# Optimization experiments

Measured on AMD Instinct MI355X. Metric: run time of the kernel, lower is better.

Reference implementation:

```python
import jax, jax.numpy as jnp
import numpy as np
import math

SEQ_LEN = 2048
DIM = 4096
N_HEADS = 32
N_KV_HEADS = 8
HEAD_DIM = DIM // N_HEADS  # 128
ROPE_THETA = 500000.0
W_SCALE = 0.02


def _precompute_freqs(head_dim, end, theta=ROPE_THETA):
    freq = 1.0 / theta ** (jnp.arange(0, head_dim, 2, dtype=jnp.float32) / head_dim)  # [hd/2]
    t = jnp.arange(end, dtype=jnp.float32)
    f = t[:, None] * freq[None, :]  # [S, hd/2]
    return jnp.cos(f), jnp.sin(f)


def _apply_rope(x, cos, sin):
    # x: [S, H, hd]; interleaved even/odd rotation, matching torch ::2 / 1::2 indexing
    xe = x[:, :, 0::2]
    xo = x[:, :, 1::2]
    c = cos[:, None, :]  # [S, 1, hd/2]
    s = sin[:, None, :]
    re = xe * c - xo * s
    ro = xe * s + xo * c
    # re-interleave: out[..., 2i] = re[..., i], out[..., 2i+1] = ro[..., i]
    return jnp.stack([re, ro], axis=-1).reshape(x.shape)


def setup_inputs() -> dict:
    key = jax.random.key(0)
    k = jax.random.split(key, 5)
    x = jax.random.normal(k[0], (SEQ_LEN, DIM), dtype=jnp.float32)
    wq = jax.random.normal(k[1], (DIM, DIM), dtype=jnp.float32) * W_SCALE
    wk = jax.random.normal(k[2], (N_KV_HEADS * HEAD_DIM, DIM), dtype=jnp.float32) * W_SCALE
    wv = jax.random.normal(k[3], (N_KV_HEADS * HEAD_DIM, DIM), dtype=jnp.float32) * W_SCALE
    wo = jax.random.normal(k[4], (DIM, DIM), dtype=jnp.float32) * W_SCALE
    return {"x": x, "wq": wq, "wk": wk, "wv": wv, "wo": wo}


def reference(x, wq, wk, wv, wo):
    S = SEQ_LEN
    rep = N_HEADS // N_KV_HEADS  # 4

    Q = (x @ wq.T).reshape(S, N_HEADS, HEAD_DIM)
    K = (x @ wk.T).reshape(S, N_KV_HEADS, HEAD_DIM)
    V = (x @ wv.T).reshape(S, N_KV_HEADS, HEAD_DIM)

    cos, sin = _precompute_freqs(HEAD_DIM, S)
    Q = _apply_rope(Q, cos, sin)
    K = _apply_rope(K, cos, sin)

    # GQA: repeat_interleave(K, rep, dim=1) maps query head h -> kv group h // rep.
    # Express natively with a grouped einsum instead of materializing repeated K/V.
    Qg = Q.transpose(1, 0, 2).reshape(N_KV_HEADS, rep, S, HEAD_DIM)  # [g, r, S, d]
    Kt = K.transpose(1, 0, 2)  # [g, S, d]
    Vt = V.transpose(1, 0, 2)  # [g, S, d]

    scores = jnp.einsum('grqd,gkd->grqk', Qg, Kt) / math.sqrt(HEAD_DIM)
    mask = jnp.triu(jnp.full((S, S), -jnp.inf, dtype=scores.dtype), k=1)
    probs = jax.nn.softmax(scores + mask, axis=-1)
    out = jnp.einsum('grqk,gkd->grqd', probs, Vt)  # [g, r, S, d]

    out = out.reshape(N_HEADS, S, HEAD_DIM).transpose(1, 0, 2).reshape(S, N_HEADS * HEAD_DIM)
    return out @ wo.T
```

## Files before the change

### kernel.cpp

```cpp
#include <hip/hip_runtime.h>

typedef unsigned short u16;
typedef short short8 __attribute__((ext_vector_type(8)));
typedef float f32x4 __attribute__((ext_vector_type(4)));
typedef unsigned short u16x4 __attribute__((ext_vector_type(4)));

typedef short8 short8_a __attribute__((may_alias));
typedef f32x4 f32x4_a __attribute__((may_alias));
typedef u16x4 u16x4_a __attribute__((may_alias));
typedef unsigned int uint_a __attribute__((may_alias));

__device__ __forceinline__ u16 f2b(float f) {
  unsigned u = __float_as_uint(f);
  u += 0x7FFFu + ((u >> 16) & 1u);
  return (u16)(u >> 16);
}

__device__ __forceinline__ void mfma_b(f32x4& d, short8 a, short8 b) {
  asm("v_mfma_f32_16x16x32_bf16 %0, %1, %2, %0" : "+v"(d) : "v"(a), "v"(b));
}

__device__ __forceinline__ void guard4(f32x4& a, f32x4& b, f32x4& c, f32x4& d) {
  asm volatile("s_nop 7\n\ts_nop 7" : "+v"(a), "+v"(b), "+v"(c), "+v"(d));
}
__device__ __forceinline__ void guard8(f32x4* o) {
  asm volatile("s_nop 7\n\ts_nop 7"
               : "+v"(o[0]), "+v"(o[1]), "+v"(o[2]), "+v"(o[3]),
                 "+v"(o[4]), "+v"(o[5]), "+v"(o[6]), "+v"(o[7]));
}

__device__ __forceinline__ void gload16(const void* g, void* l) {
  __builtin_amdgcn_global_load_lds((__attribute__((address_space(1))) void*)(g),
                                   (__attribute__((address_space(3))) void*)(l),
                                   16, 0, 0);
}

__device__ __forceinline__ void bar_v0() {
  asm volatile("s_waitcnt vmcnt(0)\n\ts_barrier" ::: "memory");
}
__device__ __forceinline__ void bar_v3() {
  asm volatile("s_waitcnt vmcnt(3)\n\ts_barrier" ::: "memory");
}

__global__ __launch_bounds__(256)
void k_prep(const float* __restrict__ x, const float* __restrict__ wq,
            const float* __restrict__ wk, const float* __restrict__ wv,
            const float* __restrict__ wo, u16* __restrict__ xb,
            u16* __restrict__ wB, u16* __restrict__ wob,
            float* __restrict__ cost, float* __restrict__ sint) {
  const long i = (long)blockIdx.x * 256 + threadIdx.x;
  const float* src;
  u16* dst;
  long j;
  if (i < 6291456) {
    if (i < 2097152) { src = x; dst = xb; j = i; }
    else { src = wq; dst = wB; j = i - 2097152; }
  } else if (i < 8388608) {
    if (i < 7340032) { src = wk; dst = wB + 16777216; j = i - 6291456; }
    else { src = wv; dst = wB + 20971520; j = i - 7340032; }
  } else if (i < 12582912) {
    src = wo; dst = wob; j = i - 8388608;
  } else {
    long ti = i - 12582912;
    int s = (int)(ti >> 6), jj = (int)(ti & 63);
    float freq = powf(500000.0f, -(float)jj * (1.0f / 64.0f));
    float a = (float)s * freq;
    float sv, cv;
    sincosf(a, &sv, &cv);
    cost[ti] = cv;
    sint[ti] = sv;
    return;
  }
  f32x4 v = ((const f32x4_a*)src)[j];
  u16x4 o;
  o[0] = f2b(v[0]); o[1] = f2b(v[1]); o[2] = f2b(v[2]); o[3] = f2b(v[3]);
  ((u16x4_a*)dst)[j] = o;
}

#define QK_SCALE 0.08838834764831845f
__global__ __launch_bounds__(512, 2)
void k_gemm8(const u16* __restrict__ A, const u16* __restrict__ B,
             const float* __restrict__ cost, const float* __restrict__ sint,
             u16* __restrict__ Qb, u16* __restrict__ Kb, u16* __restrict__ Vt) {
  extern __shared__ u16 lds[];
  const int K = 4096;
  const int tid = threadIdx.x;
  const int w = tid >> 6, lane = tid & 63;
  const int hi = lane >> 4, lo = lane & 15;
  const int wr = w >> 2, wc = w & 3;
  int bid = blockIdx.x;
  bid = (bid & 7) * 24 + (bid >> 3);
  const int tm = bid / 24, tn = bid - (bid / 24) * 24;
  const int m0 = tm << 8, n0 = tn << 8;

  const int kx = (((tid & 7) ^ ((tid >> 3) & 7)) << 3);
  const int r3 = tid >> 3;

  f32x4 acc[8][4] = {};
  short8 afr[4][2], bfr[4][2];

  const int sA0 = (wr * 128 + lo) * 64;
  const int sB0 = (wc * 64 + lo) * 64;
  const int sl0 = ((0 * 4 + hi) ^ (lo & 7)) * 8;
  const int sl1 = ((1 * 4 + hi) ^ (lo & 7)) * 8;

#define STAGE_A(sbuf, h, kt)                                                    \
  {                                                                             \
    _Pragma("unroll") for (int l = 0; l < 2; ++l) {                             \
      gload16(A + (long)(m0 + (h)*128 + l * 64 + r3) * K + (kt)*64 + kx,        \
              lds + (sbuf)*16384 + ((h)*128 + l * 64 + w * 8) * 64);            \
    }                                                                           \
  }
#define STAGE_B(sbuf, h, kt)                                                    \
  {                                                                             \
    _Pragma("unroll") for (int l = 0; l < 2; ++l) {                             \
      gload16(B + (long)(n0 + (h)*128 + l * 64 + r3) * K + (kt)*64 + kx,        \
              lds + 32768 + (sbuf)*16384 + ((h)*128 + l * 64 + w * 8) * 64);    \
    }                                                                           \
  }

  STAGE_A(0, 0, 0); STAGE_A(0, 1, 0);
  STAGE_B(0, 0, 0); STAGE_B(0, 1, 0);
  bar_v0();

  const int NI = K >> 7;
#define HALF_ITER(buf, stile, sbuf, dostage)                                    \
  {                                                                             \
    const u16* Ab_ = lds + (buf)*16384;                                         \
    const u16* Bb_ = lds + 32768 + (buf)*16384;                                 \
    if (dostage) { STAGE_A(sbuf, 0, stile); STAGE_A(sbuf, 1, stile); }          \
    _Pragma("unroll") for (int fn = 0; fn < 4; ++fn) {                          \
      bfr[fn][0] = *(const short8_a*)(Bb_ + sB0 + fn * 1024 + sl0);             \
      bfr[fn][1] = *(const short8_a*)(Bb_ + sB0 + fn * 1024 + sl1);             \
    }                                                                           \
    _Pragma("unroll") for (int fm = 0; fm < 4; ++fm) {                          \
      afr[fm][0] = *(const short8_a*)(Ab_ + sA0 + fm * 1024 + sl0);             \
      afr[fm][1] = *(const short8_a*)(Ab_ + sA0 + fm * 1024 + sl1);             \
    }                                                                           \
    __builtin_amdgcn_s_setprio(1);                                              \
    _Pragma("unroll") for (int fm = 0; fm < 4; ++fm)                            \
      _Pragma("unroll") for (int fn = 0; fn < 4; ++fn) {                        \
        mfma_b(acc[fm][fn], afr[fm][0], bfr[fn][0]);                            \
        mfma_b(acc[fm][fn], afr[fm][1], bfr[fn][1]);                            \
      }                                                                         \
    __builtin_amdgcn_s_setprio(0);                                              \
    if (dostage) { STAGE_B(sbuf, 0, stile); STAGE_B(sbuf, 1, stile); }          \
    _Pragma("unroll") for (int fm = 0; fm < 4; ++fm) {                          \
      afr[fm][0] = *(const short8_a*)(Ab_ + sA0 + (fm + 4) * 1024 + sl0);       \
      afr[fm][1] = *(const short8_a*)(Ab_ + sA0 + (fm + 4) * 1024 + sl1);       \
    }                                                                           \
    __builtin_amdgcn_s_setprio(1);                                              \
    _Pragma("unroll") for (int fm = 0; fm < 4; ++fm)                            \
      _Pragma("unroll") for (int fn = 0; fn < 4; ++fn) {                        \
        mfma_b(acc[fm + 4][fn], afr[fm][0], bfr[fn][0]);                        \
        mfma_b(acc[fm + 4][fn], afr[fm][1], bfr[fn][1]);                        \
      }                                                                         \
    __builtin_amdgcn_s_setprio(0);                                              \
    bar_v0();                                                                   \
  }

  for (int it = 0; it < NI; ++it) {
    HALF_ITER(0, 2 * it + 1, 1, true);
    HALF_ITER(1, 2 * it + 2, 0, (it + 1 < NI));
  }

  guard8(&acc[0][0]); guard8(&acc[2][0]); guard8(&acc[4][0]); guard8(&acc[6][0]);

  if (n0 < 5120) {
    const bool isQ = (n0 < 4096);
#pragma unroll
    for (int fm = 0; fm < 8; ++fm) {
      const int row0 = m0 + wr * 128 + fm * 16 + hi * 4;
#pragma unroll
      for (int fn = 0; fn < 4; ++fn) {
        const int c = n0 + wc * 64 + fn * 16 + lo;
        const int j0 = (c & 127) >> 1;
        const bool even = ((c & 1) == 0);
#pragma unroll
        for (int r = 0; r < 4; ++r) {
          float own = acc[fm][fn][r];
          float part = __shfl_xor(own, 1);
          const int s_ = row0 + r;
          const float cv = cost[s_ * 64 + j0];
          const float sv = sint[s_ * 64 + j0];
          float res = even ? (own * cv - part * sv) : (part * sv + own * cv);
          if (isQ)
            Qb[(long)s_ * 4096 + c] = f2b(res * QK_SCALE);
          else
            Kb[(long)s_ * 1024 + (c - 4096)] = f2b(res);
        }
      }
    }
  } else {
#pragma unroll
    for (int fm = 0; fm < 8; ++fm) {
      const int row0 = m0 + wr * 128 + fm * 16 + hi * 4;
#pragma unroll
      for (int fn = 0; fn < 4; ++fn) {
        const int vc = n0 - 5120 + wc * 64 + fn * 16 + lo;
        u16x4 pk;
#pragma unroll
        for (int r = 0; r < 4; ++r) pk[r] = f2b(acc[fm][fn][r]);
        *(u16x4_a*)(Vt + (long)vc * 2048 + row0) = pk;
      }
    }
  }
#undef HALF_ITER
#undef STAGE_A
#undef STAGE_B
}

__global__ __launch_bounds__(512, 2)
void k_gemm_t2(const u16* __restrict__ A, const u16* __restrict__ B,
               float* __restrict__ C) {
  extern __shared__ u16 lds2[];
  u16* As = lds2;
  u16* Bs = lds2 + 12288;
  const int K = 4096, N = 4096;
  const int tid = threadIdx.x;
  const int w = tid >> 6, lane = tid & 63;
  const int hi = lane >> 4, lo = lane & 15;
  const int wr = w >> 2, wc = w & 3;
  int bid = blockIdx.x;
  bid = (bid & 7) * 32 + (bid >> 3);
  const int tm = bid >> 4, tn = bid & 15;
  const int m0 = tm << 7, n0 = tn << 8;

  const int r2 = tid >> 2;
  const int ks = (((tid & 3) ^ ((tid >> 3) & 3)) << 3);
  const u16* Ag = A + (long)(m0 + r2) * K + ks;
  const u16* Bg0 = B + (long)(n0 + r2) * K + ks;
  const u16* Bg1 = B + (long)(n0 + 128 + r2) * K + ks;
  const int sb = w * 512;

  f32x4 acc[4][4] = {};
  const int hs = hi ^ ((lo >> 1) & 3);
  const int aoff = (wr * 64 + lo) * 32 + hs * 8;
  const int boff = (wc * 64 + lo) * 32 + hs * 8;

  const int nt = K >> 5;
  int i0 = 0, i1 = 1, i2 = 2;

#define STG2(kt, bi)                                      \
  {                                                       \
    gload16(Ag + (kt)*32, As + (bi)*4096 + sb);           \
    gload16(Bg0 + (kt)*32, Bs + (bi)*8192 + sb);          \
    gload16(Bg1 + (kt)*32, Bs + (bi)*8192 + 4096 + sb);   \
  }

  STG2(0, 0);
  STG2(1, 1);
  bar_v3();

  for (int t = 0; t < nt; ++t) {
    if (t + 2 < nt) STG2(t + 2, i2);
    short8 af[4], bf[4];
#pragma unroll
    for (int m = 0; m < 4; ++m)
      af[m] = *(const short8_a*)(As + i0 * 4096 + aoff + m * 512);
#pragma unroll
    for (int n = 0; n < 4; ++n)
      bf[n] = *(const short8_a*)(Bs + i0 * 8192 + boff + n * 512);
    __builtin_amdgcn_s_setprio(1);
#pragma unroll
    for (int m = 0; m < 4; ++m)
#pragma unroll
      for (int n = 0; n < 4; ++n) mfma_b(acc[m][n], af[m], bf[n]);
    __builtin_amdgcn_s_setprio(0);
    if (t + 2 < nt) bar_v3();
    else bar_v0();
    const int tmp = i0; i0 = i1; i1 = i2; i2 = tmp;
  }
#undef STG2
  guard8(&acc[0][0]);
  guard8(&acc[2][0]);

#pragma unroll
  for (int m = 0; m < 4; ++m) {
    const int row0 = m0 + wr * 64 + m * 16 + hi * 4;
#pragma unroll
    for (int n = 0; n < 4; ++n) {
      const int col = n0 + wc * 64 + n * 16 + lo;
#pragma unroll
      for (int r = 0; r < 4; ++r)
        C[(long)(row0 + r) * N + col] = acc[m][n][r];
    }
  }
}

#define KLD 136
#define VLD 72
__global__ __launch_bounds__(256, 2)
void k_attn(const u16* __restrict__ Qb, const u16* __restrict__ Kb,
            const u16* __restrict__ Vt, u16* __restrict__ Ab) {
  __shared__ u16 Ks[64 * KLD];
  __shared__ u16 Vs[128 * VLD];
  __shared__ u16 Ps[4 * 16 * VLD];

  const int tid = threadIdx.x;
  const int w = tid >> 6, lane = tid & 63;
  const int hi = lane >> 4, lo = lane & 15;
  const int qt = 31 - (blockIdx.x >> 5);
  const int h = blockIdx.x & 31;
  const int hkv = h >> 2;
  const int q0 = qt * 64;
  const int qrow = q0 + w * 16 + lo;

  short8 qf[4];
#pragma unroll
  for (int c = 0; c < 4; ++c)
    qf[c] = *(const short8_a*)(Qb + (long)qrow * 4096 + h * 128 + c * 32 + hi * 8);

  f32x4 o[8] = {};
  float m_run = -1e30f, l_run = 0.f;
  u16* Pw = Ps + w * (16 * VLD);

  const int ntiles = qt + 1;
  for (int t = 0; t < ntiles; ++t) {
    const int kv0 = t * 64;
    __syncthreads();
#pragma unroll
    for (int r = 0; r < 4; ++r) {
      int i = r * 256 + tid;
      int key = i >> 4, d8 = (i & 15) * 8;
      short8 v = *(const short8_a*)(Kb + (long)(kv0 + key) * 1024 + hkv * 128 + d8);
      *(short8_a*)(Ks + key * KLD + d8) = v;
    }
#pragma unroll
    for (int r = 0; r < 4; ++r) {
      int i = r * 256 + tid;
      int dd = i >> 3, k8 = (i & 7) * 8;
      short8 v = *(const short8_a*)(Vt + (long)hkv * 262144 + (long)dd * 2048 + kv0 + k8);
      *(short8_a*)(Vs + dd * VLD + k8) = v;
    }
    __syncthreads();

    f32x4 sc[4] = {};
#pragma unroll
    for (int c = 0; c < 4; ++c) {
#pragma unroll
      for (int kt = 0; kt < 4; ++kt) {
        short8 kf = *(const short8_a*)(Ks + (kt * 16 + lo) * KLD + c * 32 + hi * 8);
        mfma_b(sc[kt], kf, qf[c]);
      }
    }
    guard4(sc[0], sc[1], sc[2], sc[3]);

    if (t == ntiles - 1) {
#pragma unroll
      for (int kt = 0; kt < 4; ++kt)
#pragma unroll
        for (int r = 0; r < 4; ++r) {
          int key = kv0 + kt * 16 + hi * 4 + r;
          if (key > qrow) sc[kt][r] = -1e30f;
        }
    }
    float tmax = -1e30f;
#pragma unroll
    for (int kt = 0; kt < 4; ++kt)
#pragma unroll
      for (int r = 0; r < 4; ++r) tmax = fmaxf(tmax, sc[kt][r]);
    tmax = fmaxf(tmax, __shfl_xor(tmax, 16));
    tmax = fmaxf(tmax, __shfl_xor(tmax, 32));
    float m_new = fmaxf(m_run, tmax);
    float scale = __expf(m_run - m_new);
    float psum = 0.f;
    float p[16];
#pragma unroll
    for (int kt = 0; kt < 4; ++kt)
#pragma unroll
      for (int r = 0; r < 4; ++r) {
        float pv = __expf(sc[kt][r] - m_new);
        p[kt * 4 + r] = pv;
        psum += pv;
      }
    psum += __shfl_xor(psum, 16);
    psum += __shfl_xor(psum, 32);
    l_run = l_run * scale + psum;
    m_run = m_new;
    float srow[4];
#pragma unroll
    for (int r = 0; r < 4; ++r) srow[r] = __shfl(scale, hi * 4 + r);
#pragma unroll
    for (int n = 0; n < 8; ++n)
#pragma unroll
      for (int r = 0; r < 4; ++r) o[n][r] *= srow[r];
#pragma unroll
    for (int kt = 0; kt < 4; ++kt) {
      unsigned p01 = (unsigned)f2b(p[kt * 4]) | ((unsigned)f2b(p[kt * 4 + 1]) << 16);
      unsigned p23 = (unsigned)f2b(p[kt * 4 + 2]) | ((unsigned)f2b(p[kt * 4 + 3]) << 16);
      *(uint_a*)(Pw + lo * VLD + kt * 16 + hi * 4) = p01;
      *(uint_a*)(Pw + lo * VLD + kt * 16 + hi * 4 + 2) = p23;
    }
    __syncthreads();
#pragma unroll
    for (int c = 0; c < 2; ++c) {
      short8 pf = *(const short8_a*)(Pw + lo * VLD + c * 32 + hi * 8);
#pragma unroll
      for (int n = 0; n < 8; ++n) {
        short8 vf = *(const short8_a*)(Vs + (n * 16 + lo) * VLD + c * 32 + hi * 8);
        mfma_b(o[n], pf, vf);
      }
    }
  }
  guard8(o);

  float inv = 1.0f / l_run;
  float irow[4];
#pragma unroll
  for (int r = 0; r < 4; ++r) irow[r] = __shfl(inv, hi * 4 + r);
#pragma unroll
  for (int n = 0; n < 8; ++n)
#pragma unroll
    for (int r = 0; r < 4; ++r) {
      int q = q0 + w * 16 + hi * 4 + r;
      Ab[(long)q * 4096 + h * 128 + n * 16 + lo] = f2b(o[n][r] * irow[r]);
    }
}

extern "C" void kernel_launch(void* const* d_in, const int* in_sizes, int n_in,
                              void* d_out, int out_size, void* d_ws, size_t ws_size,
                              hipStream_t stream) {
  const float* x = (const float*)d_in[0];
  const float* wq = (const float*)d_in[1];
  const float* wk = (const float*)d_in[2];
  const float* wv = (const float*)d_in[3];
  const float* wo = (const float*)d_in[4];
  float* out = (float*)d_out;
  char* ws = (char*)d_ws;

  size_t off = 0;
  u16* xb = (u16*)(ws + off); off += 16777216;
  u16* wB = (u16*)(ws + off); off += 50331648;
  u16* wob = (u16*)(ws + off); off += 33554432;
  u16* Qb = (u16*)(ws + off); off += 16777216;
  u16* Kb = (u16*)(ws + off); off += 4194304;
  u16* Vtb = (u16*)(ws + off); off += 4194304;
  float* cost = (float*)(ws + off); off += 524288;
  float* sint = (float*)(ws + off); off += 524288;
  u16* Ab = (u16*)(ws + off); off += 16777216;

  static bool attr_set = false;
  if (!attr_set) {
    hipFuncSetAttribute((const void*)k_gemm8,
                        hipFuncAttributeMaxDynamicSharedMemorySize, 131072);
    hipFuncSetAttribute((const void*)k_gemm_t2,
                        hipFuncAttributeMaxDynamicSharedMemorySize, 73728);
    attr_set = true;
  }

  k_prep<<<49664, 256, 0, stream>>>(x, wq, wk, wv, wo, xb, wB, wob, cost, sint);

  k_gemm8<<<192, 512, 131072, stream>>>(xb, wB, cost, sint, Qb, Kb, Vtb);

  k_attn<<<1024, 256, 0, stream>>>(Qb, Kb, Vtb, Ab);

  k_gemm_t2<<<256, 512, 73728, stream>>>(Ab, wob, out);
}
```

Baseline: 350.6 us.

## Use 128x256 triple-buffered QKV GEMM and move wo conversion into attention kernel

Replaces the 256x256 double-buffered QKV projection GEMM with a 128x256 tile, K-step 32, triple-buffered variant. This doubles the block count to 384 and uses less LDS. The fp32-to-bf16 conversion of wo moves out of the prep kernel and into the start of the attention kernel, so that bandwidth-bound work can overlap with attention compute instead of running serially. The risks are lower per-block data reuse in the GEMM and slightly longer attention blocks.

```diff
diff --git a/kernel.cpp b/kernel.cpp
--- a/kernel.cpp
+++ b/kernel.cpp
@@ -45,8 +45,7 @@
 __global__ __launch_bounds__(256)
 void k_prep(const float* __restrict__ x, const float* __restrict__ wq,
             const float* __restrict__ wk, const float* __restrict__ wv,
-            const float* __restrict__ wo, u16* __restrict__ xb,
-            u16* __restrict__ wB, u16* __restrict__ wob,
+            u16* __restrict__ xb, u16* __restrict__ wB,
             float* __restrict__ cost, float* __restrict__ sint) {
   const long i = (long)blockIdx.x * 256 + threadIdx.x;
   const float* src;
@@ -58,10 +57,8 @@
   } else if (i < 8388608) {
     if (i < 7340032) { src = wk; dst = wB + 16777216; j = i - 6291456; }
     else { src = wv; dst = wB + 20971520; j = i - 7340032; }
-  } else if (i < 12582912) {
-    src = wo; dst = wob; j = i - 8388608;
   } else {
-    long ti = i - 12582912;
+    long ti = i - 8388608;
     int s = (int)(ti >> 6), jj = (int)(ti & 63);
     float freq = powf(500000.0f, -(float)jj * (1.0f / 64.0f));
     float a = (float)s * freq;
@@ -79,106 +76,84 @@
 
 #define QK_SCALE 0.08838834764831845f
 __global__ __launch_bounds__(512, 2)
-void k_gemm8(const u16* __restrict__ A, const u16* __restrict__ B,
+void k_gemmQ(const u16* __restrict__ A, const u16* __restrict__ B,
              const float* __restrict__ cost, const float* __restrict__ sint,
              u16* __restrict__ Qb, u16* __restrict__ Kb, u16* __restrict__ Vt) {
-  extern __shared__ u16 lds[];
+  extern __shared__ u16 ldsq[];
+  u16* As = ldsq;
+  u16* Bs = ldsq + 12288;
   const int K = 4096;
   const int tid = threadIdx.x;
   const int w = tid >> 6, lane = tid & 63;
   const int hi = lane >> 4, lo = lane & 15;
   const int wr = w >> 2, wc = w & 3;
   int bid = blockIdx.x;
-  bid = (bid & 7) * 24 + (bid >> 3);
+  bid = (bid & 7) * 48 + (bid >> 3);
   const int tm = bid / 24, tn = bid - (bid / 24) * 24;
-  const int m0 = tm << 8, n0 = tn << 8;
-
-  const int kx = (((tid & 7) ^ ((tid >> 3) & 7)) << 3);
-  const int r3 = tid >> 3;
-
-  f32x4 acc[8][4] = {};
-  short8 afr[4][2], bfr[4][2];
-
-  const int sA0 = (wr * 128 + lo) * 64;
-  const int sB0 = (wc * 64 + lo) * 64;
-  const int sl0 = ((0 * 4 + hi) ^ (lo & 7)) * 8;
-  const int sl1 = ((1 * 4 + hi) ^ (lo & 7)) * 8;
-
-#define STAGE_A(sbuf, h, kt)                                                    \
-  {                                                                             \
-    _Pragma("unroll") for (int l = 0; l < 2; ++l) {                             \
-      gload16(A + (long)(m0 + (h)*128 + l * 64 + r3) * K + (kt)*64 + kx,        \
-              lds + (sbuf)*16384 + ((h)*128 + l * 64 + w * 8) * 64);            \
-    }                                                                           \
-  }
-#define STAGE_B(sbuf, h, kt)                                                    \
-  {                                                                             \
-    _Pragma("unroll") for (int l = 0; l < 2; ++l) {                             \
-      gload16(B + (long)(n0 + (h)*128 + l * 64 + r3) * K + (kt)*64 + kx,        \
-              lds + 32768 + (sbuf)*16384 + ((h)*128 + l * 64 + w * 8) * 64);    \
-    }                                                                           \
-  }
-
-  STAGE_A(0, 0, 0); STAGE_A(0, 1, 0);
-  STAGE_B(0, 0, 0); STAGE_B(0, 1, 0);
-  bar_v0();
-
-  const int NI = K >> 7;
-#define HALF_ITER(buf, stile, sbuf, dostage)                                    \
-  {                                                                             \
-    const u16* Ab_ = lds + (buf)*16384;                                         \
-    const u16* Bb_ = lds + 32768 + (buf)*16384;                                 \
-    if (dostage) { STAGE_A(sbuf, 0, stile); STAGE_A(sbuf, 1, stile); }          \
-    _Pragma("unroll") for (int fn = 0; fn < 4; ++fn) {                          \
-      bfr[fn][0] = *(const short8_a*)(Bb_ + sB0 + fn * 1024 + sl0);             \
-      bfr[fn][1] = *(const short8_a*)(Bb_ + sB0 + fn * 1024 + sl1);             \
-    }                                                                           \
-    _Pragma("unroll") for (int fm = 0; fm < 4; ++fm) {                          \
-      afr[fm][0] = *(const short8_a*)(Ab_ + sA0 + fm * 1024 + sl0);             \
-      afr[fm][1] = *(const short8_a*)(Ab_ + sA0 + fm * 1024 + sl1);             \
-    }                                                                           \
-    __builtin_amdgcn_s_setprio(1);                                              \
-    _Pragma("unroll") for (int fm = 0; fm < 4; ++fm)                            \
-      _Pragma("unroll") for (int fn = 0; fn < 4; ++fn) {                        \
-        mfma_b(acc[fm][fn], afr[fm][0], bfr[fn][0]);                            \
-        mfma_b(acc[fm][fn], afr[fm][1], bfr[fn][1]);                            \
-      }                                                                         \
-    __builtin_amdgcn_s_setprio(0);                                              \
-    if (dostage) { STAGE_B(sbuf, 0, stile); STAGE_B(sbuf, 1, stile); }          \
-    _Pragma("unroll") for (int fm = 0; fm < 4; ++fm) {                          \
-      afr[fm][0] = *(const short8_a*)(Ab_ + sA0 + (fm + 4) * 1024 + sl0);       \
-      afr[fm][1] = *(const short8_a*)(Ab_ + sA0 + (fm + 4) * 1024 + sl1);       \
-    }                                                                           \
-    __builtin_amdgcn_s_setprio(1);                                              \
-    _Pragma("unroll") for (int fm = 0; fm < 4; ++fm)                            \
-      _Pragma("unroll") for (int fn = 0; fn < 4; ++fn) {                        \
-        mfma_b(acc[fm + 4][fn], afr[fm][0], bfr[fn][0]);                        \
-        mfma_b(acc[fm + 4][fn], afr[fm][1], bfr[fn][1]);                        \
-      }                                                                         \
-    __builtin_amdgcn_s_setprio(0);                                              \
-    bar_v0();                                                                   \
-  }
-
-  for (int it = 0; it < NI; ++it) {
-    HALF_ITER(0, 2 * it + 1, 1, true);
-    HALF_ITER(1, 2 * it + 2, 0, (it + 1 < NI));
-  }
-
-  guard8(&acc[0][0]); guard8(&acc[2][0]); guard8(&acc[4][0]); guard8(&acc[6][0]);
+  const int m0 = tm << 7, n0 = tn << 8;
+
+  const int r2 = tid >> 2;
+  const int ks = (((tid & 3) ^ ((tid >> 3) & 3)) << 3);
+  const u16* Ag = A + (long)(m0 + r2) * K + ks;
+  const u16* Bg0 = B + (long)(n0 + r2) * K + ks;
+  const u16* Bg1 = B + (long)(n0 + 128 + r2) * K + ks;
+  const int sb = w * 512;
+
+  f32x4 acc[4][4] = {};
+  const int hs = hi ^ ((lo >> 1) & 3);
+  const int aoff = (wr * 64 + lo) * 32 + hs * 8;
+  const int boff = (wc * 64 + lo) * 32 + hs * 8;
+
+  const int nt = K >> 5;
+  int i0 = 0, i1 = 1, i2 = 2;
+
+#define STGQ(kt, bi)                                      \
+  {                                                       \
+    gload16(Ag + (kt)*32, As + (bi)*4096 + sb);           \
+    gload16(Bg0 + (kt)*32, Bs + (bi)*8192 + sb);          \
+    gload16(Bg1 + (kt)*32, Bs + (bi)*8192 + 4096 + sb);   \
+  }
+
+  STGQ(0, 0);
+  STGQ(1, 1);
+  bar_v3();
+
+  for (int t = 0; t < nt; ++t) {
+    if (t + 2 < nt) STGQ(t + 2, i2);
+    short8 af[4], bf[4];
+#pragma unroll
+    for (int m = 0; m < 4; ++m)
+      af[m] = *(const short8_a*)(As + i0 * 4096 + aoff + m * 512);
+#pragma unroll
+    for (int n = 0; n < 4; ++n)
+      bf[n] = *(const short8_a*)(Bs + i0 * 8192 + boff + n * 512);
+    __builtin_amdgcn_s_setprio(1);
+#pragma unroll
+    for (int m = 0; m < 4; ++m)
+#pragma unroll
+      for (int n = 0; n < 4; ++n) mfma_b(acc[m][n], af[m], bf[n]);
+    __builtin_amdgcn_s_setprio(0);
+    if (t + 2 < nt) bar_v3();
+    else bar_v0();
+    const int tmp = i0; i0 = i1; i1 = i2; i2 = tmp;
+  }
+#undef STGQ
+  guard8(&acc[0][0]);
+  guard8(&acc[2][0]);
 
   if (n0 < 5120) {
     const bool isQ = (n0 < 4096);
 #pragma unroll
-    for (int fm = 0; fm < 8; ++fm) {
-      const int row0 = m0 + wr * 128 + fm * 16 + hi * 4;
-#pragma unroll
-      for (int fn = 0; fn < 4; ++fn) {
-        const int c = n0 + wc * 64 + fn * 16 + lo;
+    for (int m = 0; m < 4; ++m) {
+      const int row0 = m0 + wr * 64 + m * 16 + hi * 4;
+#pragma unroll
+      for (int n = 0; n < 4; ++n) {
+        const int c = n0 + wc * 64 + n * 16 + lo;
         const int j0 = (c & 127) >> 1;
         const bool even = ((c & 1) == 0);
 #pragma unroll
         for (int r = 0; r < 4; ++r) {
-          float own = acc[fm][fn][r];
+          float own = acc[m][n][r];
           float part = __shfl_xor(own, 1);
           const int s_ = row0 + r;
           const float cv = cost[s_ * 64 + j0];
@@ -193,21 +168,18 @@
     }
   } else {
 #pragma unroll
-    for (int fm = 0; fm < 8; ++fm) {
-      const int row0 = m0 + wr * 128 + fm * 16 + hi * 4;
-#pragma unroll
-      for (int fn = 0; fn < 4; ++fn) {
-        const int vc = n0 - 5120 + wc * 64 + fn * 16 + lo;
+    for (int m = 0; m < 4; ++m) {
+      const int row0 = m0 + wr * 64 + m * 16 + hi * 4;
+#pragma unroll
+      for (int n = 0; n < 4; ++n) {
+        const int vc = n0 - 5120 + wc * 64 + n * 16 + lo;
         u16x4 pk;
 #pragma unroll
-        for (int r = 0; r < 4; ++r) pk[r] = f2b(acc[fm][fn][r]);
+        for (int r = 0; r < 4; ++r) pk[r] = f2b(acc[m][n][r]);
         *(u16x4_a*)(Vt + (long)vc * 2048 + row0) = pk;
       }
     }
   }
-#undef HALF_ITER
-#undef STAGE_A
-#undef STAGE_B
 }
 
 __global__ __launch_bounds__(512, 2)
@@ -292,7 +264,20 @@
 #define VLD 72
 __global__ __launch_bounds__(256, 2)
 void k_attn(const u16* __restrict__ Qb, const u16* __restrict__ Kb,
-            const u16* __restrict__ Vt, u16* __restrict__ Ab) {
+            const u16* __restrict__ Vt, u16* __restrict__ Ab,
+            const float* __restrict__ wo, u16* __restrict__ wob) {
+  {
+    const long base = (long)blockIdx.x * 256 + threadIdx.x;
+#pragma unroll
+    for (int c = 0; c < 16; ++c) {
+      const long idx = base + (long)c * 262144;
+      f32x4 v = ((const f32x4_a*)wo)[idx];
+      u16x4 o;
+      o[0] = f2b(v[0]); o[1] = f2b(v[1]); o[2] = f2b(v[2]); o[3] = f2b(v[3]);
+      ((u16x4_a*)wob)[idx] = o;
+    }
+  }
+
   __shared__ u16 Ks[64 * KLD];
   __shared__ u16 Vs[128 * VLD];
   __shared__ u16 Ps[4 * 16 * VLD];
@@ -442,18 +427,18 @@
 
   static bool attr_set = false;
   if (!attr_set) {
-    hipFuncSetAttribute((const void*)k_gemm8,
-                        hipFuncAttributeMaxDynamicSharedMemorySize, 131072);
+    hipFuncSetAttribute((const void*)k_gemmQ,
+                        hipFuncAttributeMaxDynamicSharedMemorySize, 73728);
     hipFuncSetAttribute((const void*)k_gemm_t2,
                         hipFuncAttributeMaxDynamicSharedMemorySize, 73728);
     attr_set = true;
   }
 
-  k_prep<<<49664, 256, 0, stream>>>(x, wq, wk, wv, wo, xb, wB, wob, cost, sint);
-
-  k_gemm8<<<192, 512, 131072, stream>>>(xb, wB, cost, sint, Qb, Kb, Vtb);
-
-  k_attn<<<1024, 256, 0, stream>>>(Qb, Kb, Vtb, Ab);
+  k_prep<<<33280, 256, 0, stream>>>(x, wq, wk, wv, xb, wB, cost, sint);
+
+  k_gemmQ<<<384, 512, 73728, stream>>>(xb, wB, cost, sint, Qb, Kb, Vtb);
+
+  k_attn<<<1024, 256, 0, stream>>>(Qb, Kb, Vtb, Ab, wo, wob);
 
   k_gemm_t2<<<256, 512, 73728, stream>>>(Ab, wob, out);
 }
```

Result: slower. 372.4 us (+6.2%).

## Restructure QKV GEMM mainloop into 4-stage K=32 pipeline with deeper prefetch

Applied to the files above, without the earlier changes.

Replaces the double-buffered K=64 mainloop of the fused QKV projection GEMM with a 4-buffer ring of K=32 tiles, prefetching three tiles ahead. Each wait now uses a partial vmcnt instead of draining all loads, so more global-to-LDS traffic stays in flight during MFMA work. The LDS swizzle changes to suit 32-element rows, and the launch bound drops to one block per CU. In exchange, barriers happen twice as often per unit of K, and there are fewer MFMAs per barrier.

```diff
diff --git a/kernel.cpp b/kernel.cpp
--- a/kernel.cpp
+++ b/kernel.cpp
@@ -40,6 +40,12 @@
 }
 __device__ __forceinline__ void bar_v3() {
   asm volatile("s_waitcnt vmcnt(3)\n\ts_barrier" ::: "memory");
+}
+__device__ __forceinline__ void bar_v4() {
+  asm volatile("s_waitcnt vmcnt(4)\n\ts_barrier" ::: "memory");
+}
+__device__ __forceinline__ void bar_v8() {
+  asm volatile("s_waitcnt vmcnt(8)\n\ts_barrier" ::: "memory");
 }
 
 __global__ __launch_bounds__(256)
@@ -78,11 +84,13 @@
 }
 
 #define QK_SCALE 0.08838834764831845f
-__global__ __launch_bounds__(512, 2)
-void k_gemm8(const u16* __restrict__ A, const u16* __restrict__ B,
+__global__ __launch_bounds__(512, 1)
+void k_gemmX(const u16* __restrict__ A, const u16* __restrict__ B,
              const float* __restrict__ cost, const float* __restrict__ sint,
              u16* __restrict__ Qb, u16* __restrict__ Kb, u16* __restrict__ Vt) {
-  extern __shared__ u16 lds[];
+  extern __shared__ u16 ldsx[];
+  u16* As = ldsx;
+  u16* Bs = ldsx + 32768;
   const int K = 4096;
   const int tid = threadIdx.x;
   const int w = tid >> 6, lane = tid & 63;
@@ -93,76 +101,55 @@
   const int tm = bid / 24, tn = bid - (bid / 24) * 24;
   const int m0 = tm << 8, n0 = tn << 8;
 
-  const int kx = (((tid & 7) ^ ((tid >> 3) & 7)) << 3);
-  const int r3 = tid >> 3;
+  const int r2 = tid >> 2;
+  const int ks = (((tid & 3) ^ ((tid >> 3) & 3)) << 3);
+  const u16* Ag0 = A + (long)(m0 + r2) * K + ks;
+  const u16* Ag1 = A + (long)(m0 + 128 + r2) * K + ks;
+  const u16* Bg0 = B + (long)(n0 + r2) * K + ks;
+  const u16* Bg1 = B + (long)(n0 + 128 + r2) * K + ks;
+  const int sb = w * 512;
 
   f32x4 acc[8][4] = {};
-  short8 afr[4][2], bfr[4][2];
-
-  const int sA0 = (wr * 128 + lo) * 64;
-  const int sB0 = (wc * 64 + lo) * 64;
-  const int sl0 = ((0 * 4 + hi) ^ (lo & 7)) * 8;
-  const int sl1 = ((1 * 4 + hi) ^ (lo & 7)) * 8;
-
-#define STAGE_A(sbuf, h, kt)                                                    \
-  {                                                                             \
-    _Pragma("unroll") for (int l = 0; l < 2; ++l) {                             \
-      gload16(A + (long)(m0 + (h)*128 + l * 64 + r3) * K + (kt)*64 + kx,        \
-              lds + (sbuf)*16384 + ((h)*128 + l * 64 + w * 8) * 64);            \
-    }                                                                           \
-  }
-#define STAGE_B(sbuf, h, kt)                                                    \
-  {                                                                             \
-    _Pragma("unroll") for (int l = 0; l < 2; ++l) {                             \
-      gload16(B + (long)(n0 + (h)*128 + l * 64 + r3) * K + (kt)*64 + kx,        \
-              lds + 32768 + (sbuf)*16384 + ((h)*128 + l * 64 + w * 8) * 64);    \
-    }                                                                           \
-  }
-
-  STAGE_A(0, 0, 0); STAGE_A(0, 1, 0);
-  STAGE_B(0, 0, 0); STAGE_B(0, 1, 0);
-  bar_v0();
-
-  const int NI = K >> 7;
-#define HALF_ITER(buf, stile, sbuf, dostage)                                    \
-  {                                                                             \
-    const u16* Ab_ = lds + (buf)*16384;                                         \
-    const u16* Bb_ = lds + 32768 + (buf)*16384;                                 \
-    if (dostage) { STAGE_A(sbuf, 0, stile); STAGE_A(sbuf, 1, stile); }          \
-    _Pragma("unroll") for (int fn = 0; fn < 4; ++fn) {                          \
-      bfr[fn][0] = *(const short8_a*)(Bb_ + sB0 + fn * 1024 + sl0);             \
-      bfr[fn][1] = *(const short8_a*)(Bb_ + sB0 + fn * 1024 + sl1);             \
-    }                                                                           \
-    _Pragma("unroll") for (int fm = 0; fm < 4; ++fm) {                          \
-      afr[fm][0] = *(const short8_a*)(Ab_ + sA0 + fm * 1024 + sl0);             \
-      afr[fm][1] = *(const short8_a*)(Ab_ + sA0 + fm * 1024 + sl1);             \
-    }                                                                           \
-    __builtin_amdgcn_s_setprio(1);                                              \
-    _Pragma("unroll") for (int fm = 0; fm < 4; ++fm)                            \
-      _Pragma("unroll") for (int fn = 0; fn < 4; ++fn) {                        \
-        mfma_b(acc[fm][fn], afr[fm][0], bfr[fn][0]);                            \
-        mfma_b(acc[fm][fn], afr[fm][1], bfr[fn][1]);                            \
-      }                                                                         \
-    __builtin_amdgcn_s_setprio(0);                                              \
-    if (dostage) { STAGE_B(sbuf, 0, stile); STAGE_B(sbuf, 1, stile); }          \
-    _Pragma("unroll") for (int fm = 0; fm < 4; ++fm) {                          \
-      afr[fm][0] = *(const short8_a*)(Ab_ + sA0 + (fm + 4) * 1024 + sl0);       \
-      afr[fm][1] = *(const short8_a*)(Ab_ + sA0 + (fm + 4) * 1024 + sl1);       \
-    }                                                                           \
-    __builtin_amdgcn_s_setprio(1);                                              \
-    _Pragma("unroll") for (int fm = 0; fm < 4; ++fm)                            \
-      _Pragma("unroll") for (int fn = 0; fn < 4; ++fn) {                        \
-        mfma_b(acc[fm + 4][fn], afr[fm][0], bfr[fn][0]);                        \
-        mfma_b(acc[fm + 4][fn], afr[fm][1], bfr[fn][1]);                        \
-      }                                                                         \
-    __builtin_amdgcn_s_setprio(0);                                              \
-    bar_v0();                                                                   \
-  }
-
-  for (int it = 0; it < NI; ++it) {
-    HALF_ITER(0, 2 * it + 1, 1, true);
-    HALF_ITER(1, 2 * it + 2, 0, (it + 1 < NI));
-  }
+  const int hs = hi ^ ((lo >> 1) & 3);
+  const int sA0 = (wr * 128 + lo) * 32 + hs * 8;
+  const int sB0 = (wc * 64 + lo) * 32 + hs * 8;
+
+  const int nt = K >> 5;
+
+#define STGX(kt, bi)                                          \
+  {                                                           \
+    gload16(Ag0 + (kt)*32, As + (bi)*8192 + sb);              \
+    gload16(Ag1 + (kt)*32, As + (bi)*8192 + 4096 + sb);       \
+    gload16(Bg0 + (kt)*32, Bs + (bi)*8192 + sb);              \
+    gload16(Bg1 + (kt)*32, Bs + (bi)*8192 + 4096 + sb);       \
+  }
+
+  STGX(0, 0); STGX(1, 1); STGX(2, 2);
+  bar_v8();
+
+  for (int t = 0; t < nt; ++t) {
+    const int cb = t & 3;
+    if (t + 3 < nt) STGX(t + 3, (t + 3) & 3);
+    const u16* Ab_ = As + cb * 8192;
+    const u16* Bb_ = Bs + cb * 8192;
+    short8 afr[8], bfr[4];
+#pragma unroll
+    for (int fn = 0; fn < 4; ++fn)
+      bfr[fn] = *(const short8_a*)(Bb_ + sB0 + fn * 512);
+#pragma unroll
+    for (int fm = 0; fm < 8; ++fm)
+      afr[fm] = *(const short8_a*)(Ab_ + sA0 + fm * 512);
+    __builtin_amdgcn_s_setprio(1);
+#pragma unroll
+    for (int fm = 0; fm < 8; ++fm)
+#pragma unroll
+      for (int fn = 0; fn < 4; ++fn) mfma_b(acc[fm][fn], afr[fm], bfr[fn]);
+    __builtin_amdgcn_s_setprio(0);
+    if (t + 3 < nt) bar_v8();
+    else if (t + 2 < nt) bar_v4();
+    else bar_v0();
+  }
+#undef STGX
 
   guard8(&acc[0][0]); guard8(&acc[2][0]); guard8(&acc[4][0]); guard8(&acc[6][0]);
 
@@ -205,9 +192,6 @@
       }
     }
   }
-#undef HALF_ITER
-#undef STAGE_A
-#undef STAGE_B
 }
 
 __global__ __launch_bounds__(512, 2)
@@ -442,7 +426,7 @@
 
   static bool attr_set = false;
   if (!attr_set) {
-    hipFuncSetAttribute((const void*)k_gemm8,
+    hipFuncSetAttribute((const void*)k_gemmX,
                         hipFuncAttributeMaxDynamicSharedMemorySize, 131072);
     hipFuncSetAttribute((const void*)k_gemm_t2,
                         hipFuncAttributeMaxDynamicSharedMemorySize, 73728);
@@ -451,7 +435,7 @@
 
   k_prep<<<49664, 256, 0, stream>>>(x, wq, wk, wv, wo, xb, wB, wob, cost, sint);
 
-  k_gemm8<<<192, 512, 131072, stream>>>(xb, wB, cost, sint, Qb, Kb, Vtb);
+  k_gemmX<<<192, 512, 131072, stream>>>(xb, wB, cost, sint, Qb, Kb, Vtb);
 
   k_attn<<<1024, 256, 0, stream>>>(Qb, Kb, Vtb, Ab);
 
```

After: 360.7 us. 2.9% more time.
